# Kernel optimization log

Measured on AMD Instinct MI355X. Metric: run time of the kernel, lower is better.

Reference implementation:

```python
import jax, jax.numpy as jnp
import numpy as np

OUT = 14          # output_size of mask_roi_pool
RATIO = 2         # sampling_ratio
SCALES = (0.25, 0.125, 0.0625, 0.03125)  # strides 4,8,16,32 for 800x800 images
CANON_SCALE = 224.0
CANON_LVL = 4.0
K_MIN = 2.0       # -log2(0.25)
K_MAX = 5.0


def setup_inputs() -> dict:
    key = jax.random.key(0)
    ks = jax.random.split(key, 8)
    B, N, C = 2, 128, 256
    feats = {}
    for i, hw in enumerate([200, 100, 50, 25]):
        feats[f"feat{i}"] = jax.random.normal(ks[i], (B, C, hw, hw), dtype=jnp.float32)
    # valid xyxy boxes in [0,800] with log-uniform sizes spanning all FPN levels
    img = 800.0
    logw = jax.random.uniform(ks[4], (B, N), minval=jnp.log(16.0), maxval=jnp.log(600.0))
    logh = jax.random.uniform(ks[5], (B, N), minval=jnp.log(16.0), maxval=jnp.log(600.0))
    w, h = jnp.exp(logw), jnp.exp(logh)
    x1 = jax.random.uniform(ks[6], (B, N)) * (img - w)
    y1 = jax.random.uniform(ks[7], (B, N)) * (img - h)
    boxes = jnp.stack([x1, y1, x1 + w, y1 + h], axis=-1).astype(jnp.float32)
    feats["boxes"] = boxes
    return feats


def _prep_axis(c, L):
    # torchvision roi_align bilinear clamp semantics (aligned=False)
    valid = (c > -1.0) & (c < L)
    c = jnp.clip(c, 0.0, L - 1.0)
    lo = jnp.clip(jnp.floor(c), 0.0, L - 2.0).astype(jnp.int32)
    frac = c - lo.astype(c.dtype)
    return valid, lo, frac


def _roi_align_level(feat, rois, bidx, scale):
    # feat: [B,C,H,W], rois: [K,4] xyxy image coords, bidx: [K] int32
    B, C, H, W = feat.shape
    K = rois.shape[0]
    x1 = rois[:, 0] * scale
    y1 = rois[:, 1] * scale
    x2 = rois[:, 2] * scale
    y2 = rois[:, 3] * scale
    rw = jnp.maximum(x2 - x1, 1.0)
    rh = jnp.maximum(y2 - y1, 1.0)
    bw = rw / OUT
    bh = rh / OUT
    # sample offsets within roi in bin units: (ph*RATIO + iy + 0.5)/RATIO, flattened [OUT*RATIO]
    off = (jnp.arange(OUT * RATIO, dtype=feat.dtype) + 0.5) / RATIO
    ys = y1[:, None] + bh[:, None] * off  # [K, 28]
    xs = x1[:, None] + bw[:, None] * off  # [K, 28]
    vy, ylo, ly = _prep_axis(ys, H)
    vx, xlo, lx = _prep_axis(xs, W)
    hy, hx = 1.0 - ly, 1.0 - lx
    feat_r = feat.transpose(0, 2, 3, 1).reshape(B * H * W, C)
    base = bidx[:, None, None] * (H * W)

    def gather(yi, xi):
        idx = base + yi[:, :, None] * W + xi[:, None, :]  # [K,28,28]
        return feat_r[idx]  # [K,28,28,C]

    val = (gather(ylo, xlo) * (hy[:, :, None] * hx[:, None, :])[..., None]
           + gather(ylo, xlo + 1) * (hy[:, :, None] * lx[:, None, :])[..., None]
           + gather(ylo + 1, xlo) * (ly[:, :, None] * hx[:, None, :])[..., None]
           + gather(ylo + 1, xlo + 1) * (ly[:, :, None] * lx[:, None, :])[..., None])
    mask = (vy[:, :, None] & vx[:, None, :])[..., None]
    val = jnp.where(mask, val, 0.0)
    # average RATIO x RATIO samples per output bin
    val = val.reshape(K, OUT, RATIO, OUT, RATIO, C).mean(axis=(2, 4))
    return val.transpose(0, 3, 1, 2)  # [K, C, OUT, OUT]


def _forward(feat0, feat1, feat2, feat3, boxes):
    feats = (feat0, feat1, feat2, feat3)
    B, N = boxes.shape[0], boxes.shape[1]
    rois = boxes.reshape(B * N, 4)
    bidx = jnp.repeat(jnp.arange(B, dtype=jnp.int32), N)
    # FPN level mapper (torchvision LevelMapper)
    w = rois[:, 2] - rois[:, 0]
    h = rois[:, 3] - rois[:, 1]
    s = jnp.sqrt(w * h)
    lvl = jnp.floor(CANON_LVL + jnp.log2(s / CANON_SCALE + 1e-6))
    lvl_idx = (jnp.clip(lvl, K_MIN, K_MAX) - K_MIN).astype(jnp.int32)  # [K] in 0..3
    per_level = jnp.stack(
        [_roi_align_level(f, rois, bidx, sc) for f, sc in zip(feats, SCALES)]
    )  # [4, K, C, 14, 14]
    K = rois.shape[0]
    return per_level[lvl_idx, jnp.arange(K)]  # [K, C, 14, 14]


def reference(feat0, feat1, feat2, feat3, boxes):
    return _forward(feat0, feat1, feat2, feat3, boxes)
```

## Files before the change

kernel.cpp:

```cpp
#include <hip/hip_runtime.h>
#include <math.h>

#define OUT 14
#define RATIO 2
#define NS (OUT*RATIO)
#define NPIX (OUT*OUT)
#define C_TOT 256
#define CG 4
#define NBOX_PER_B 128
#define NTHREADS 256
#define PATCH_CAP 1280
#define NROI 256

#define META_INTS 8
#define META_OFF  0
#define IDX_OFF   (NROI*META_INTS*4)
#define WY_OFF    (IDX_OFF + NROI*NPIX*16)
#define WX_OFF    (WY_OFF  + NROI*NPIX*16)
#define WS_NEEDED (WX_OFF  + NROI*NPIX*16)

__global__ __launch_bounds__(NTHREADS)
void roi_setup_kernel(const float* __restrict__ boxes,
                      int*    __restrict__ metaW,
                      int4*   __restrict__ idxW,
                      float4* __restrict__ wyW,
                      float4* __restrict__ wxW)
{
    const int k   = blockIdx.x;
    const int tid = threadIdx.x;

    __shared__ int   s_ylo[NS], s_xlo[NS];
    __shared__ float s_fyh[NS], s_fyl[NS], s_fxh[NS], s_fxl[NS];

    const float bx1 = boxes[k*4+0];
    const float by1 = boxes[k*4+1];
    const float bx2 = boxes[k*4+2];
    const float by2 = boxes[k*4+3];

    const float wbox = bx2 - bx1;
    const float hbox = by2 - by1;
    const float sdim = sqrtf(wbox * hbox);
    float lvlf = floorf(4.0f + log2f(sdim / 224.0f + 1e-6f));
    lvlf = fminf(fmaxf(lvlf, 2.0f), 5.0f);
    const int lidx = (int)lvlf - 2;

    int H, W;
    float scale;
    if      (lidx == 0) { H = 200; W = 200; scale = 0.25f;    }
    else if (lidx == 1) { H = 100; W = 100; scale = 0.125f;   }
    else if (lidx == 2) { H = 50;  W = 50;  scale = 0.0625f;  }
    else                { H = 25;  W = 25;  scale = 0.03125f; }

    const float x1 = bx1 * scale;
    const float y1 = by1 * scale;
    const float x2 = bx2 * scale;
    const float y2 = by2 * scale;
    const float rw = fmaxf(x2 - x1, 1.0f);
    const float rh = fmaxf(y2 - y1, 1.0f);
    const float bw = rw / (float)OUT;
    const float bh = rh / (float)OUT;

    if (tid < NS) {
        const int i = tid;
        const float off = ((float)i + 0.5f) / (float)RATIO;
        {
            const float c  = y1 + bh * off;
            const bool  v  = (c > -1.0f) && (c < (float)H);
            const float cc = fminf(fmaxf(c, 0.0f), (float)(H - 1));
            const float fl = fminf(fmaxf(floorf(cc), 0.0f), (float)(H - 2));
            const float fr = cc - fl;
            s_ylo[i] = (int)fl;
            s_fyl[i] = v ? fr         : 0.0f;
            s_fyh[i] = v ? 1.0f - fr  : 0.0f;
        }
        {
            const float c  = x1 + bw * off;
            const bool  v  = (c > -1.0f) && (c < (float)W);
            const float cc = fminf(fmaxf(c, 0.0f), (float)(W - 1));
            const float fl = fminf(fmaxf(floorf(cc), 0.0f), (float)(W - 2));
            const float fr = cc - fl;
            s_xlo[i] = (int)fl;
            s_fxl[i] = v ? fr         : 0.0f;
            s_fxh[i] = v ? 1.0f - fr  : 0.0f;
        }
    }
    __syncthreads();

    const int ymin  = s_ylo[0];
    const int xmin  = s_xlo[0];
    const int nrows = s_ylo[NS-1] + 2 - ymin;
    const int ncols = s_xlo[NS-1] + 2 - xmin;
    const int padded  = ncols | 1;
    const int stridep = (nrows * padded <= PATCH_CAP) ? padded : ncols;

    if (tid == 0) {
        int* m = metaW + k*META_INTS;
        m[0] = lidx;
        m[1] = ymin;
        m[2] = xmin;
        m[3] = nrows;
        m[4] = ncols;
        m[5] = stridep;
        m[6] = nrows * ncols;
        m[7] = __float_as_int(1.0f / (float)ncols);
    }

    if (tid < NPIX) {
        const int ph = tid / OUT;
        const int pw = tid - ph * OUT;
        const int sy0 = 2*ph, sy1 = 2*ph + 1;
        const int sx0 = 2*pw, sx1 = 2*pw + 1;
        int4 iv;
        iv.x = (s_ylo[sy0] - ymin) * stridep;
        iv.y = (s_ylo[sy1] - ymin) * stridep;
        iv.z =  s_xlo[sx0] - xmin;
        iv.w =  s_xlo[sx1] - xmin;
        idxW[k*NPIX + tid] = iv;
        float4 wy;
        wy.x = s_fyh[sy0] * 0.25f;
        wy.y = s_fyl[sy0] * 0.25f;
        wy.z = s_fyh[sy1] * 0.25f;
        wy.w = s_fyl[sy1] * 0.25f;
        float4 wx;
        wx.x = s_fxh[sx0];
        wx.y = s_fxl[sx0];
        wx.z = s_fxh[sx1];
        wx.w = s_fxl[sx1];
        wyW[k*NPIX + tid] = wy;
        wxW[k*NPIX + tid] = wx;
    }
}

__global__ __launch_bounds__(NTHREADS)
void roi_align_main_kernel(const float* __restrict__ f0,
                           const float* __restrict__ f1,
                           const float* __restrict__ f2,
                           const float* __restrict__ f3,
                           const int*    __restrict__ metaW,
                           const int4*   __restrict__ idxW,
                           const float4* __restrict__ wyW,
                           const float4* __restrict__ wxW,
                           float* __restrict__ out)
{
    const int cg  = blockIdx.x;
    const int k   = blockIdx.y;
    const int tid = threadIdx.x;

    __shared__ float4 s_patch[PATCH_CAP];

    const bool active = (tid < NPIX);
    int4   iv = {0,0,0,0};
    float4 wy = {0,0,0,0};
    float4 wx = {0,0,0,0};
    if (active) {
        iv = idxW[k*NPIX + tid];
        wy = wyW[k*NPIX + tid];
        wx = wxW[k*NPIX + tid];
    }

    const int* m = metaW + k*META_INTS;
    const int lidx    = m[0];
    const int ymin    = m[1];
    const int xmin    = m[2];
    const int ncols   = m[4];
    const int stridep = m[5];
    const int nelem   = m[6];
    const float rcpc  = __int_as_float(m[7]);

    const float* fptr;
    int W;
    if      (lidx == 0) { fptr = f0; W = 200; }
    else if (lidx == 1) { fptr = f1; W = 100; }
    else if (lidx == 2) { fptr = f2; W = 50;  }
    else                { fptr = f3; W = 25;  }
    const size_t plane = (size_t)W * (size_t)W;

    const float* fbase = fptr
        + ((size_t)(k / NBOX_PER_B) * C_TOT + (size_t)cg * CG) * plane
        + (size_t)ymin * W + xmin;
    const float* g0 = fbase;
    const float* g1 = fbase +   plane;
    const float* g2 = fbase + 2*plane;
    const float* g3 = fbase + 3*plane;

    for (int i = tid; i < nelem; i += NTHREADS) {
        const int r  = (int)(((float)i + 0.5f) * rcpc);
        const int cc = i - r * ncols;
        const int go = r * W + cc;
        const int di = r * stridep + cc;
        float4 v;
        v.x = g0[go]; v.y = g1[go]; v.z = g2[go]; v.w = g3[go];
        if (di < PATCH_CAP) s_patch[di] = v;
    }
    __syncthreads();

    if (active) {
        float4 acc = {0.0f, 0.0f, 0.0f, 0.0f};
        #pragma unroll
        for (int ys = 0; ys < 2; ++ys) {
            const int   rb = ys ? iv.y : iv.x;
            const float yh = ys ? wy.z : wy.x;
            const float yl = ys ? wy.w : wy.y;
            #pragma unroll
            for (int xs = 0; xs < 2; ++xs) {
                const int base = rb + (xs ? iv.w : iv.z);
                const float xh = xs ? wx.z : wx.x;
                const float xl = xs ? wx.w : wx.y;
                const float w00 = yh*xh, w01 = yh*xl, w10 = yl*xh, w11 = yl*xl;
                const float4 v00 = s_patch[base];
                const float4 v01 = s_patch[base + 1];
                const float4 v10 = s_patch[base + stridep];
                const float4 v11 = s_patch[base + stridep + 1];
                acc.x += w00*v00.x + w01*v01.x + w10*v10.x + w11*v11.x;
                acc.y += w00*v00.y + w01*v01.y + w10*v10.y + w11*v11.y;
                acc.z += w00*v00.z + w01*v01.z + w10*v10.z + w11*v11.z;
                acc.w += w00*v00.w + w01*v01.w + w10*v10.w + w11*v11.w;
            }
        }
        float* ob = out + ((size_t)k * C_TOT + (size_t)cg * CG) * NPIX + tid;
        ob[0*NPIX] = acc.x;
        ob[1*NPIX] = acc.y;
        ob[2*NPIX] = acc.z;
        ob[3*NPIX] = acc.w;
    }
}

__global__ __launch_bounds__(NTHREADS)
void roi_align_fpn_kernel(const float* __restrict__ f0,
                          const float* __restrict__ f1,
                          const float* __restrict__ f2,
                          const float* __restrict__ f3,
                          const float* __restrict__ boxes,
                          float* __restrict__ out)
{
    const int k   = blockIdx.x;
    const int cg  = blockIdx.y;
    const int tid = threadIdx.x;

    __shared__ float4 s_patch[PATCH_CAP];
    __shared__ int   s_ylo[NS], s_xlo[NS];
    __shared__ float s_fyh[NS], s_fyl[NS], s_fxh[NS], s_fxl[NS];

    const float bx1 = boxes[k*4+0];
    const float by1 = boxes[k*4+1];
    const float bx2 = boxes[k*4+2];
    const float by2 = boxes[k*4+3];

    const float wbox = bx2 - bx1;
    const float hbox = by2 - by1;
    const float sdim = sqrtf(wbox * hbox);
    float lvlf = floorf(4.0f + log2f(sdim / 224.0f + 1e-6f));
    lvlf = fminf(fmaxf(lvlf, 2.0f), 5.0f);
    const int lidx = (int)lvlf - 2;

    const float* fptr;
    int H, W;
    float scale;
    if      (lidx == 0) { fptr = f0; H = 200; W = 200; scale = 0.25f;    }
    else if (lidx == 1) { fptr = f1; H = 100; W = 100; scale = 0.125f;   }
    else if (lidx == 2) { fptr = f2; H = 50;  W = 50;  scale = 0.0625f;  }
    else                { fptr = f3; H = 25;  W = 25;  scale = 0.03125f; }

    const float x1 = bx1 * scale;
    const float y1 = by1 * scale;
    const float x2 = bx2 * scale;
    const float y2 = by2 * scale;
    const float rw = fmaxf(x2 - x1, 1.0f);
    const float rh = fmaxf(y2 - y1, 1.0f);
    const float bw = rw / (float)OUT;
    const float bh = rh / (float)OUT;

    if (tid < NS) {
        const int i = tid;
        const float off = ((float)i + 0.5f) / (float)RATIO;
        {
            const float c  = y1 + bh * off;
            const bool  v  = (c > -1.0f) && (c < (float)H);
            const float cc = fminf(fmaxf(c, 0.0f), (float)(H - 1));
            const float fl = fminf(fmaxf(floorf(cc), 0.0f), (float)(H - 2));
            const float fr = cc - fl;
            s_ylo[i] = (int)fl;
            s_fyl[i] = v ? fr         : 0.0f;
            s_fyh[i] = v ? 1.0f - fr  : 0.0f;
        }
        {
            const float c  = x1 + bw * off;
            const bool  v  = (c > -1.0f) && (c < (float)W);
            const float cc = fminf(fmaxf(c, 0.0f), (float)(W - 1));
            const float fl = fminf(fmaxf(floorf(cc), 0.0f), (float)(W - 2));
            const float fr = cc - fl;
            s_xlo[i] = (int)fl;
            s_fxl[i] = v ? fr         : 0.0f;
            s_fxh[i] = v ? 1.0f - fr  : 0.0f;
        }
    }
    __syncthreads();

    const int ymin  = s_ylo[0];
    const int xmin  = s_xlo[0];
    const int nrows = s_ylo[NS-1] + 2 - ymin;
    const int ncols = s_xlo[NS-1] + 2 - xmin;
    const int padded = ncols | 1;
    const int stridep = (nrows * padded <= PATCH_CAP) ? padded : ncols;
    const int nelem = nrows * ncols;
    const float rcpc = 1.0f / (float)ncols;

    const bool active = (tid < NPIX);
    int rb0 = 0, rb1 = 0, cbase0 = 0, cbase1 = 0;
    float wt[16];
    #pragma unroll
    for (int i = 0; i < 16; ++i) wt[i] = 0.0f;
    if (active) {
        const int ph = tid / OUT;
        const int pw = tid - ph * OUT;
        const int sy0 = 2*ph, sy1 = 2*ph + 1;
        const int sx0 = 2*pw, sx1 = 2*pw + 1;
        rb0 = (s_ylo[sy0] - ymin) * stridep;
        rb1 = (s_ylo[sy1] - ymin) * stridep;
        cbase0 = s_xlo[sx0] - xmin;
        cbase1 = s_xlo[sx1] - xmin;
        const float fyh_[2] = { s_fyh[sy0], s_fyh[sy1] };
        const float fyl_[2] = { s_fyl[sy0], s_fyl[sy1] };
        const float fxh_[2] = { s_fxh[sx0], s_fxh[sx1] };
        const float fxl_[2] = { s_fxl[sx0], s_fxl[sx1] };
        #pragma unroll
        for (int ys = 0; ys < 2; ++ys) {
            #pragma unroll
            for (int xs = 0; xs < 2; ++xs) {
                const int o = (ys*2 + xs) * 4;
                wt[o+0] = fyh_[ys] * fxh_[xs] * 0.25f;
                wt[o+1] = fyh_[ys] * fxl_[xs] * 0.25f;
                wt[o+2] = fyl_[ys] * fxh_[xs] * 0.25f;
                wt[o+3] = fyl_[ys] * fxl_[xs] * 0.25f;
            }
        }
    }

    const int bidx = k / NBOX_PER_B;
    const size_t plane = (size_t)H * (size_t)W;
    const float* fbase = fptr + ((size_t)bidx * C_TOT + (size_t)cg * CG) * plane
                              + (size_t)ymin * W + xmin;
    const float* g0 = fbase;
    const float* g1 = fbase + plane;
    const float* g2 = fbase + 2*plane;
    const float* g3 = fbase + 3*plane;
    for (int i = tid; i < nelem; i += NTHREADS) {
        const int r  = (int)(((float)i + 0.5f) * rcpc);
        const int cc = i - r * ncols;
        const int go = r * W + cc;
        const int di = r * stridep + cc;
        float4 v;
        v.x = g0[go]; v.y = g1[go]; v.z = g2[go]; v.w = g3[go];
        if (di < PATCH_CAP) s_patch[di] = v;
    }
    __syncthreads();

    if (active) {
        float4 acc = {0.0f, 0.0f, 0.0f, 0.0f};
        #pragma unroll
        for (int ys = 0; ys < 2; ++ys) {
            const int rbase = (ys == 0) ? rb0 : rb1;
            #pragma unroll
            for (int xs = 0; xs < 2; ++xs) {
                const int base = rbase + ((xs == 0) ? cbase0 : cbase1);
                const float4 v00 = s_patch[base];
                const float4 v01 = s_patch[base + 1];
                const float4 v10 = s_patch[base + stridep];
                const float4 v11 = s_patch[base + stridep + 1];
                const int o = (ys*2 + xs) * 4;
                const float w00 = wt[o+0], w01 = wt[o+1], w10 = wt[o+2], w11 = wt[o+3];
                acc.x += w00*v00.x + w01*v01.x + w10*v10.x + w11*v11.x;
                acc.y += w00*v00.y + w01*v01.y + w10*v10.y + w11*v11.y;
                acc.z += w00*v00.z + w01*v01.z + w10*v10.z + w11*v11.z;
                acc.w += w00*v00.w + w01*v01.w + w10*v10.w + w11*v11.w;
            }
        }
        float* ob = out + ((size_t)k * C_TOT + (size_t)cg * CG) * NPIX + tid;
        ob[0*NPIX] = acc.x;
        ob[1*NPIX] = acc.y;
        ob[2*NPIX] = acc.z;
        ob[3*NPIX] = acc.w;
    }
}

extern "C" void kernel_launch(void* const* d_in, const int* in_sizes, int n_in,
                              void* d_out, int out_size, void* d_ws, size_t ws_size,
                              hipStream_t stream) {
    const float* f0    = (const float*)d_in[0];
    const float* f1    = (const float*)d_in[1];
    const float* f2    = (const float*)d_in[2];
    const float* f3    = (const float*)d_in[3];
    const float* boxes = (const float*)d_in[4];
    float* out = (float*)d_out;

    if (ws_size >= (size_t)WS_NEEDED) {
        char* ws = (char*)d_ws;
        int*    metaW = (int*)   (ws + META_OFF);
        int4*   idxW  = (int4*)  (ws + IDX_OFF);
        float4* wyW   = (float4*)(ws + WY_OFF);
        float4* wxW   = (float4*)(ws + WX_OFF);

        roi_setup_kernel<<<NROI, NTHREADS, 0, stream>>>(boxes, metaW, idxW, wyW, wxW);
        dim3 grid(C_TOT / CG, NROI);
        roi_align_main_kernel<<<grid, NTHREADS, 0, stream>>>(
            f0, f1, f2, f3, metaW, idxW, wyW, wxW, out);
    } else {
        dim3 grid(NROI, C_TOT / CG);
        roi_align_fpn_kernel<<<grid, NTHREADS, 0, stream>>>(f0, f1, f2, f3, boxes, out);
    }
}
```

Before: 43.20 us.

## Process four channel groups per block with register-prefetched patch loads

The main kernel now has each block handle four consecutive groups of four channels instead of one, looping over them. It precomputes gather offsets once, and while computing the current group from shared memory it prefetches the next group's patch into registers, overlapping global loads with compute. This removes per-block index and weight reloads and adds latency hiding. The cost is a grid four times smaller with more registers per thread, which may reduce occupancy. The fixed MAXIT=5 bound caps the patch at 1280 elements, the same as PATCH_CAP.

```diff
diff --git a/kernel.cpp b/kernel.cpp
--- a/kernel.cpp
+++ b/kernel.cpp
@@ -7,9 +7,12 @@
 #define NPIX (OUT*OUT)
 #define C_TOT 256
 #define CG 4
+#define GPB 4
+#define NCHUNK (C_TOT/(CG*GPB))
 #define NBOX_PER_B 128
 #define NTHREADS 256
 #define PATCH_CAP 1280
+#define MAXIT 5
 #define NROI 256
 
 #define META_INTS 8
@@ -132,7 +135,7 @@
 }
 
 __global__ __launch_bounds__(NTHREADS)
-void roi_align_main_kernel(const float* __restrict__ f0,
+void roi_align_pipe_kernel(const float* __restrict__ f0,
                            const float* __restrict__ f1,
                            const float* __restrict__ f2,
                            const float* __restrict__ f3,
@@ -142,9 +145,9 @@
                            const float4* __restrict__ wxW,
                            float* __restrict__ out)
 {
-    const int cg  = blockIdx.x;
-    const int k   = blockIdx.y;
-    const int tid = threadIdx.x;
+    const int chunk = blockIdx.x;
+    const int k     = blockIdx.y;
+    const int tid   = threadIdx.x;
 
     __shared__ float4 s_patch[PATCH_CAP];
 
@@ -176,52 +179,85 @@
     const size_t plane = (size_t)W * (size_t)W;
 
     const float* fbase = fptr
-        + ((size_t)(k / NBOX_PER_B) * C_TOT + (size_t)cg * CG) * plane
+        + ((size_t)(k / NBOX_PER_B) * C_TOT + (size_t)chunk * (GPB*CG)) * plane
         + (size_t)ymin * W + xmin;
-    const float* g0 = fbase;
-    const float* g1 = fbase +   plane;
-    const float* g2 = fbase + 2*plane;
-    const float* g3 = fbase + 3*plane;
-
-    for (int i = tid; i < nelem; i += NTHREADS) {
+
+    int go_[MAXIT], di_[MAXIT];
+    #pragma unroll
+    for (int t = 0; t < MAXIT; ++t) {
+        const int i  = t*NTHREADS + tid;
         const int r  = (int)(((float)i + 0.5f) * rcpc);
         const int cc = i - r * ncols;
-        const int go = r * W + cc;
-        const int di = r * stridep + cc;
-        float4 v;
-        v.x = g0[go]; v.y = g1[go]; v.z = g2[go]; v.w = g3[go];
-        if (di < PATCH_CAP) s_patch[di] = v;
-    }
-    __syncthreads();
-
-    if (active) {
-        float4 acc = {0.0f, 0.0f, 0.0f, 0.0f};
+        go_[t] = r * W + cc;
+        di_[t] = (i < nelem) ? (r * stridep + cc) : -1;
+    }
+
+    float4 sv[MAXIT];
+    {
+        const float* g0 = fbase;
         #pragma unroll
-        for (int ys = 0; ys < 2; ++ys) {
-            const int   rb = ys ? iv.y : iv.x;
-            const float yh = ys ? wy.z : wy.x;
-            const float yl = ys ? wy.w : wy.y;
+        for (int t = 0; t < MAXIT; ++t) {
+            if (di_[t] >= 0) {
+                const int go = go_[t];
+                sv[t].x = g0[go];
+                sv[t].y = g0[go +   plane];
+                sv[t].z = g0[go + 2*plane];
+                sv[t].w = g0[go + 3*plane];
+            }
+        }
+    }
+
+    #pragma unroll
+    for (int g = 0; g < GPB; ++g) {
+        #pragma unroll
+        for (int t = 0; t < MAXIT; ++t)
+            if (di_[t] >= 0) s_patch[di_[t]] = sv[t];
+
+        if (g + 1 < GPB) {
+            const float* gN = fbase + (size_t)((g+1)*CG) * plane;
             #pragma unroll
-            for (int xs = 0; xs < 2; ++xs) {
-                const int base = rb + (xs ? iv.w : iv.z);
-                const float xh = xs ? wx.z : wx.x;
-                const float xl = xs ? wx.w : wx.y;
-                const float w00 = yh*xh, w01 = yh*xl, w10 = yl*xh, w11 = yl*xl;
-                const float4 v00 = s_patch[base];
-                const float4 v01 = s_patch[base + 1];
-                const float4 v10 = s_patch[base + stridep];
-                const float4 v11 = s_patch[base + stridep + 1];
-                acc.x += w00*v00.x + w01*v01.x + w10*v10.x + w11*v11.x;
-                acc.y += w00*v00.y + w01*v01.y + w10*v10.y + w11*v11.y;
-                acc.z += w00*v00.z + w01*v01.z + w10*v10.z + w11*v11.z;
-                acc.w += w00*v00.w + w01*v01.w + w10*v10.w + w11*v11.w;
+            for (int t = 0; t < MAXIT; ++t) {
+                if (di_[t] >= 0) {
+                    const int go = go_[t];
+                    sv[t].x = gN[go];
+                    sv[t].y = gN[go +   plane];
+                    sv[t].z = gN[go + 2*plane];
+                    sv[t].w = gN[go + 3*plane];
+                }
             }
         }
-        float* ob = out + ((size_t)k * C_TOT + (size_t)cg * CG) * NPIX + tid;
-        ob[0*NPIX] = acc.x;
-        ob[1*NPIX] = acc.y;
-        ob[2*NPIX] = acc.z;
-        ob[3*NPIX] = acc.w;
+        __syncthreads();
+
+        if (active) {
+            float4 acc = {0.0f, 0.0f, 0.0f, 0.0f};
+            #pragma unroll
+            for (int ys = 0; ys < 2; ++ys) {
+                const int   rb = ys ? iv.y : iv.x;
+                const float yh = ys ? wy.z : wy.x;
+                const float yl = ys ? wy.w : wy.y;
+                #pragma unroll
+                for (int xs = 0; xs < 2; ++xs) {
+                    const int base = rb + (xs ? iv.w : iv.z);
+                    const float xh = xs ? wx.z : wx.x;
+                    const float xl = xs ? wx.w : wx.y;
+                    const float w00 = yh*xh, w01 = yh*xl, w10 = yl*xh, w11 = yl*xl;
+                    const float4 v00 = s_patch[base];
+                    const float4 v01 = s_patch[base + 1];
+                    const float4 v10 = s_patch[base + stridep];
+                    const float4 v11 = s_patch[base + stridep + 1];
+                    acc.x += w00*v00.x + w01*v01.x + w10*v10.x + w11*v11.x;
+                    acc.y += w00*v00.y + w01*v01.y + w10*v10.y + w11*v11.y;
+                    acc.z += w00*v00.z + w01*v01.z + w10*v10.z + w11*v11.z;
+                    acc.w += w00*v00.w + w01*v01.w + w10*v10.w + w11*v11.w;
+                }
+            }
+            float* ob = out + ((size_t)k * C_TOT + (size_t)(chunk*GPB + g) * CG) * NPIX + tid;
+            ob[0*NPIX] = acc.x;
+            ob[1*NPIX] = acc.y;
+            ob[2*NPIX] = acc.z;
+            ob[3*NPIX] = acc.w;
+        }
+        __syncthreads();
     }
 }
 
@@ -401,8 +437,8 @@
         float4* wxW   = (float4*)(ws + WX_OFF);
 
         roi_setup_kernel<<<NROI, NTHREADS, 0, stream>>>(boxes, metaW, idxW, wyW, wxW);
-        dim3 grid(C_TOT / CG, NROI);
-        roi_align_main_kernel<<<grid, NTHREADS, 0, stream>>>(
+        dim3 grid(NCHUNK, NROI);
+        roi_align_pipe_kernel<<<grid, NTHREADS, 0, stream>>>(
             f0, f1, f2, f3, metaW, idxW, wyW, wxW, out);
     } else {
         dim3 grid(NROI, C_TOT / CG);
```

Result: no change. 43.77 us (+1.3%).

## Use separable two-pass bilinear interpolation through shared memory

Applied to the files above, without the earlier changes.

Splits the 2D bilinear sampling and averaging into two separable passes. The first pass reduces along the shorter patch axis into a shared intermediate buffer, and the second pass combines along the other axis per output bin. The goal is fewer shared-memory float4 reads and FMAs per output than the 16-tap direct gather. In exchange it adds a second barrier, extra shared memory that may cut occupancy, and a cap on the intermediate buffer that could truncate results for very large patches.

```diff
diff --git a/kernel.cpp b/kernel.cpp
--- a/kernel.cpp
+++ b/kernel.cpp
@@ -10,6 +10,7 @@
 #define NBOX_PER_B 128
 #define NTHREADS 256
 #define PATCH_CAP 1280
+#define CRED_CAP 512
 #define NROI 256
 
 #define META_INTS 8
@@ -111,42 +112,47 @@
         const int sy0 = 2*ph, sy1 = 2*ph + 1;
         const int sx0 = 2*pw, sx1 = 2*pw + 1;
         int4 iv;
-        iv.x = (s_ylo[sy0] - ymin) * stridep;
-        iv.y = (s_ylo[sy1] - ymin) * stridep;
-        iv.z =  s_xlo[sx0] - xmin;
-        iv.w =  s_xlo[sx1] - xmin;
+        iv.x = s_ylo[sy0] - ymin;
+        iv.y = s_ylo[sy1] - ymin;
+        iv.z = s_xlo[sx0] - xmin;
+        iv.w = s_xlo[sx1] - xmin;
         idxW[k*NPIX + tid] = iv;
         float4 wy;
-        wy.x = s_fyh[sy0] * 0.25f;
-        wy.y = s_fyl[sy0] * 0.25f;
-        wy.z = s_fyh[sy1] * 0.25f;
-        wy.w = s_fyl[sy1] * 0.25f;
+        wy.x = s_fyh[sy0] * 0.5f;
+        wy.y = s_fyl[sy0] * 0.5f;
+        wy.z = s_fyh[sy1] * 0.5f;
+        wy.w = s_fyl[sy1] * 0.5f;
         float4 wx;
-        wx.x = s_fxh[sx0];
-        wx.y = s_fxl[sx0];
-        wx.z = s_fxh[sx1];
-        wx.w = s_fxl[sx1];
+        wx.x = s_fxh[sx0] * 0.5f;
+        wx.y = s_fxl[sx0] * 0.5f;
+        wx.z = s_fxh[sx1] * 0.5f;
+        wx.w = s_fxl[sx1] * 0.5f;
         wyW[k*NPIX + tid] = wy;
         wxW[k*NPIX + tid] = wx;
     }
 }
 
 __global__ __launch_bounds__(NTHREADS)
-void roi_align_main_kernel(const float* __restrict__ f0,
-                           const float* __restrict__ f1,
-                           const float* __restrict__ f2,
-                           const float* __restrict__ f3,
-                           const int*    __restrict__ metaW,
-                           const int4*   __restrict__ idxW,
-                           const float4* __restrict__ wyW,
-                           const float4* __restrict__ wxW,
-                           float* __restrict__ out)
+void roi_align_sep_kernel(const float* __restrict__ f0,
+                          const float* __restrict__ f1,
+                          const float* __restrict__ f2,
+                          const float* __restrict__ f3,
+                          const int*    __restrict__ metaW,
+                          const int4*   __restrict__ idxW,
+                          const float4* __restrict__ wyW,
+                          const float4* __restrict__ wxW,
+                          float* __restrict__ out)
 {
     const int cg  = blockIdx.x;
     const int k   = blockIdx.y;
     const int tid = threadIdx.x;
 
     __shared__ float4 s_patch[PATCH_CAP];
+    __shared__ float4 s_cred[CRED_CAP];
+    __shared__ int2   s_xcb[OUT];
+    __shared__ float4 s_xw[OUT];
+    __shared__ int2   s_yrb[OUT];
+    __shared__ float4 s_yw[OUT];
 
     const bool active = (tid < NPIX);
     int4   iv = {0,0,0,0};
@@ -162,10 +168,12 @@
     const int lidx    = m[0];
     const int ymin    = m[1];
     const int xmin    = m[2];
+    const int nrows   = m[3];
     const int ncols   = m[4];
     const int stridep = m[5];
     const int nelem   = m[6];
     const float rcpc  = __int_as_float(m[7]);
+    const bool yfirst = (nrows <= ncols);
 
     const float* fptr;
     int W;
@@ -174,6 +182,16 @@
     else if (lidx == 2) { fptr = f2; W = 50;  }
     else                { fptr = f3; W = 25;  }
     const size_t plane = (size_t)W * (size_t)W;
+
+    if (tid < OUT) {
+        s_xcb[tid] = make_int2(iv.z, iv.w);
+        s_xw[tid]  = wx;
+    }
+    if (active && (tid % OUT) == 0) {
+        const int ph = tid / OUT;
+        s_yrb[ph] = make_int2(iv.x, iv.y);
+        s_yw[ph]  = wy;
+    }
 
     const float* fbase = fptr
         + ((size_t)(k / NBOX_PER_B) * C_TOT + (size_t)cg * CG) * plane
@@ -194,29 +212,65 @@
     }
     __syncthreads();
 
+    const int ntask1 = yfirst ? nrows * OUT : OUT * ncols;
+    for (int t = tid; t < ntask1; t += NTHREADS) {
+        float4 acc;
+        if (yfirst) {
+            const int r  = t / OUT;
+            const int pw = t - r * OUT;
+            const int2   cb = s_xcb[pw];
+            const float4 w  = s_xw[pw];
+            const float4* P = s_patch + r * stridep;
+            const float4 vA = P[cb.x];
+            const float4 vB = P[cb.x + 1];
+            const float4 vC = P[cb.y];
+            const float4 vD = P[cb.y + 1];
+            acc.x = w.x*vA.x + w.y*vB.x + w.z*vC.x + w.w*vD.x;
+            acc.y = w.x*vA.y + w.y*vB.y + w.z*vC.y + w.w*vD.y;
+            acc.z = w.x*vA.z + w.y*vB.z + w.z*vC.z + w.w*vD.z;
+            acc.w = w.x*vA.w + w.y*vB.w + w.z*vC.w + w.w*vD.w;
+        } else {
+            const int ph = (int)(((float)t + 0.5f) * rcpc);
+            const int c  = t - ph * ncols;
+            const int2   rb = s_yrb[ph];
+            const float4 w  = s_yw[ph];
+            const float4 vA = s_patch[ rb.x      * stridep + c];
+            const float4 vB = s_patch[(rb.x + 1) * stridep + c];
+            const float4 vC = s_patch[ rb.y      * stridep + c];
+            const float4 vD = s_patch[(rb.y + 1) * stridep + c];
+            acc.x = w.x*vA.x + w.y*vB.x + w.z*vC.x + w.w*vD.x;
+            acc.y = w.x*vA.y + w.y*vB.y + w.z*vC.y + w.w*vD.y;
+            acc.z = w.x*vA.z + w.y*vB.z + w.z*vC.z + w.w*vD.z;
+            acc.w = w.x*vA.w + w.y*vB.w + w.z*vC.w + w.w*vD.w;
+        }
+        if (t < CRED_CAP) s_cred[t] = acc;
+    }
+    __syncthreads();
+
     if (active) {
-        float4 acc = {0.0f, 0.0f, 0.0f, 0.0f};
-        #pragma unroll
-        for (int ys = 0; ys < 2; ++ys) {
-            const int   rb = ys ? iv.y : iv.x;
-            const float yh = ys ? wy.z : wy.x;
-            const float yl = ys ? wy.w : wy.y;
-            #pragma unroll
-            for (int xs = 0; xs < 2; ++xs) {
-                const int base = rb + (xs ? iv.w : iv.z);
-                const float xh = xs ? wx.z : wx.x;
-                const float xl = xs ? wx.w : wx.y;
-                const float w00 = yh*xh, w01 = yh*xl, w10 = yl*xh, w11 = yl*xl;
-                const float4 v00 = s_patch[base];
-                const float4 v01 = s_patch[base + 1];
-                const float4 v10 = s_patch[base + stridep];
-                const float4 v11 = s_patch[base + stridep + 1];
-                acc.x += w00*v00.x + w01*v01.x + w10*v10.x + w11*v11.x;
-                acc.y += w00*v00.y + w01*v01.y + w10*v10.y + w11*v11.y;
-                acc.z += w00*v00.z + w01*v01.z + w10*v10.z + w11*v11.z;
-                acc.w += w00*v00.w + w01*v01.w + w10*v10.w + w11*v11.w;
-            }
-        }
+        const int ph = tid / OUT;
+        const int pw = tid - ph * OUT;
+        float4 vA, vB, vC, vD, w;
+        if (yfirst) {
+            vA = s_cred[ iv.x      * OUT + pw];
+            vB = s_cred[(iv.x + 1) * OUT + pw];
+            vC = s_cred[ iv.y      * OUT + pw];
+            vD = s_cred[(iv.y + 1) * OUT + pw];
+            w  = wy;
+        } else {
+            const int rbase = ph * ncols;
+            vA = s_cred[rbase + iv.z];
+            vB = s_cred[rbase + iv.z + 1];
+            vC = s_cred[rbase + iv.w];
+            vD = s_cred[rbase + iv.w + 1];
+            w  = wx;
+        }
+        float4 acc;
+        acc.x = w.x*vA.x + w.y*vB.x + w.z*vC.x + w.w*vD.x;
+        acc.y = w.x*vA.y + w.y*vB.y + w.z*vC.y + w.w*vD.y;
+        acc.z = w.x*vA.z + w.y*vB.z + w.z*vC.z + w.w*vD.z;
+        acc.w = w.x*vA.w + w.y*vB.w + w.z*vC.w + w.w*vD.w;
+
         float* ob = out + ((size_t)k * C_TOT + (size_t)cg * CG) * NPIX + tid;
         ob[0*NPIX] = acc.x;
         ob[1*NPIX] = acc.y;
@@ -402,7 +456,7 @@
 
         roi_setup_kernel<<<NROI, NTHREADS, 0, stream>>>(boxes, metaW, idxW, wyW, wxW);
         dim3 grid(C_TOT / CG, NROI);
-        roi_align_main_kernel<<<grid, NTHREADS, 0, stream>>>(
+        roi_align_sep_kernel<<<grid, NTHREADS, 0, stream>>>(
             f0, f1, f2, f3, metaW, idxW, wyW, wxW, out);
     } else {
         dim3 grid(NROI, C_TOT / CG);
```

Measured after the change: 49.77 us. 15.2% more time.
